# Performance work log

Hardware: AMD Instinct MI355X
Metric: run time of the kernel (lower is better)

## Reference

```python
import jax, jax.numpy as jnp
import numpy as np

N, C = 131072, 1000
ALPHA_LINK = 0.25  # weight applied when pred is a 'linked' (acceptable) confusion of gt
GAMMA = 2.0        # focal exponent


def setup_inputs() -> dict:
    key = jax.random.key(0)
    k1, k2, k3, k4 = jax.random.split(key, 4)
    y_pred = jax.random.normal(k1, (N, C), dtype=jnp.float32)
    y_true = jax.random.randint(k2, (N,), 0, C, dtype=jnp.int64)
    # Dense representation of the python link dict: link_matrix[gt, pred] == True
    # iff pred is in link[gt]; has_link[gt] == True iff gt is a key of link.
    link_matrix = jax.random.bernoulli(k3, 0.01, (C, C))
    has_link = jax.random.bernoulli(k4, 0.5, (C,))
    return {"y_pred": y_pred, "y_true": y_true,
            "link_matrix": link_matrix, "has_link": has_link}


def reference(y_pred, y_true, link_matrix, has_link):
    # per-sample cross entropy (stable log-softmax + gather)
    logp = jax.nn.log_softmax(y_pred, axis=-1)                     # [N, C]
    ce = -jnp.take_along_axis(logp, y_true[:, None], axis=1)[:, 0]  # [N]
    pt = jnp.exp(-ce)                                              # [N]
    pred = jnp.argmax(y_pred, axis=1)                              # [N]
    # link_bad: ALPHA_LINK iff pred != gt, gt in link, and pred in link[gt]; else 1
    linked = link_matrix[y_true, pred] & has_link[y_true] & (pred != y_true)
    w = jnp.where(linked, jnp.float32(ALPHA_LINK), jnp.float32(1.0))
    return jnp.mean(w * (1.0 - pt) ** GAMMA * ce)
```

## Files before the change

### kernel.cpp

```cpp
#include <hip/hip_runtime.h>
#include <math.h>


#define NROWS 131072
#define NC 1000
#define NF4 250
#define ROWS_PER_WAVE 4
#define WAVES_PER_BLOCK 4
#define ROWS_PER_BLOCK (ROWS_PER_WAVE * WAVES_PER_BLOCK)
#define NBLOCKS (NROWS / ROWS_PER_BLOCK)
#define NWAVES (NBLOCKS * WAVES_PER_BLOCK)
#define ALPHA_LINK 0.25f

__device__ __forceinline__ void load_row(const float4* __restrict__ rowp,
                                         int lane, float4 v[4]) {
    v[0] = rowp[lane];
    v[1] = rowp[lane + 64];
    v[2] = rowp[lane + 128];
    v[3] = (lane + 192 < NF4) ? rowp[lane + 192]
         : make_float4(-INFINITY, -INFINITY, -INFINITY, -INFINITY);
}

__global__ __launch_bounds__(256) void lfl_main(
    const float* __restrict__ yp,
    const int* __restrict__ yt,
    const unsigned char* __restrict__ linkb, const int* __restrict__ linki,
    const unsigned char* __restrict__ hasb,  const int* __restrict__ hasi,
    const unsigned int* __restrict__ hlw,
    float* __restrict__ partial)
{
    const int lane  = threadIdx.x & 63;
    const int wid   = threadIdx.x >> 6;
    const int gwave = blockIdx.x * WAVES_PER_BLOCK + wid;

    const int hi = yt[2 * lane + 1];
    const int y64 = (__ballot(hi != 0) == 0ULL);
    const unsigned int h0 = hlw[lane];
    const unsigned int h1 = hlw[lane + 64];
    const unsigned int h2 = hlw[lane + 128];
    const unsigned int h3 = (lane + 192 < NF4) ? hlw[lane + 192] : 0u;
    const int bfmt = (__ballot((h0 > 1u) | (h1 > 1u) | (h2 > 1u) | (h3 > 1u)) != 0ULL);

    const int row0 = blockIdx.x * ROWS_PER_BLOCK + wid * ROWS_PER_WAVE;
    float wsum = 0.0f;

    float4 v[4];
    load_row((const float4*)(yp + (size_t)row0 * NC), lane, v);

    #pragma unroll
    for (int r = 0; r < ROWS_PER_WAVE; ++r) {
        const int row = row0 + r;
        const int target = y64 ? yt[2 * row] : yt[row];
        const int tf = target >> 2;
        const int tl = target & 3;

        float4 vn[4];
        if (r + 1 < ROWS_PER_WAVE)
            load_row((const float4*)(yp + (size_t)(row + 1) * NC), lane, vn);

        float m = -INFINITY;
        int   idx = 1 << 30;
        float xt = 0.0f;
        #pragma unroll
        for (int k = 0; k < 4; ++k) {
            const int f  = lane + 64 * k;
            const int c0 = f * 4;
            const float x0 = v[k].x, x1 = v[k].y, x2 = v[k].z, x3 = v[k].w;
            if (x0 > m) { m = x0; idx = c0; }
            if (x1 > m) { m = x1; idx = c0 + 1; }
            if (x2 > m) { m = x2; idx = c0 + 2; }
            if (x3 > m) { m = x3; idx = c0 + 3; }
            if (f == tf) xt = (tl == 0) ? x0 : (tl == 1) ? x1 : (tl == 2) ? x2 : x3;
        }

        float s = 0.0f;
        #pragma unroll
        for (int k = 0; k < 4; ++k) {
            s += __expf(v[k].x - m) + __expf(v[k].y - m)
               + __expf(v[k].z - m) + __expf(v[k].w - m);
        }

        const float xts = __shfl(xt, tf & 63);

        #pragma unroll
        for (int off = 32; off; off >>= 1) {
            const float om = __shfl_xor(m, off);
            const int   oi = __shfl_xor(idx, off);
            const float os = __shfl_xor(s, off);
            const float mn = fmaxf(m, om);
            s = s * __expf(m - mn) + os * __expf(om - mn);
            if (om > m || (om == m && oi < idx)) idx = oi;
            m = mn;
        }

        const float logp_t = xts - m - __logf(s);
        const float ce = -logp_t;
        const float pt = __expf(logp_t);
        const int pred = idx;

        const size_t ofs = (size_t)target * NC + (size_t)pred;
        const bool lm = bfmt ? (linkb[ofs] != 0)    : (linki[ofs] != 0);
        const bool hb = bfmt ? (hasb[target] != 0)  : (hasi[target] != 0);
        const float w = (lm && hb && (pred != target)) ? ALPHA_LINK : 1.0f;

        const float ompt = 1.0f - pt;
        wsum += w * ompt * ompt * ce;

        if (r + 1 < ROWS_PER_WAVE) {
            v[0] = vn[0]; v[1] = vn[1]; v[2] = vn[2]; v[3] = vn[3];
        }
    }

    if (lane == 0) partial[gwave] = wsum;
}

__global__ __launch_bounds__(1024) void lfl_final(const float* __restrict__ partial,
                                                  float* __restrict__ out) {
    __shared__ float sm[1024];
    float s = 0.0f;
    for (int i = threadIdx.x; i < NWAVES; i += 1024) s += partial[i];
    sm[threadIdx.x] = s;
    __syncthreads();
    for (int stride = 512; stride; stride >>= 1) {
        if ((int)threadIdx.x < stride) sm[threadIdx.x] += sm[threadIdx.x + stride];
        __syncthreads();
    }
    if (threadIdx.x == 0) out[0] = sm[0] * (1.0f / (float)NROWS);
}

extern "C" void kernel_launch(void* const* d_in, const int* in_sizes, int n_in,
                              void* d_out, int out_size, void* d_ws, size_t ws_size,
                              hipStream_t stream) {
    const float* yp = (const float*)d_in[0];
    const int*   yt = (const int*)d_in[1];
    const void*  lk = d_in[2];
    const void*  hl = d_in[3];

    float* partial = (float*)d_ws;

    lfl_main<<<NBLOCKS, 256, 0, stream>>>(
        yp, yt,
        (const unsigned char*)lk, (const int*)lk,
        (const unsigned char*)hl, (const int*)hl,
        (const unsigned int*)hl,
        partial);
    lfl_final<<<1, 1024, 0, stream>>>(partial, (float*)d_out);
}
```

Measured before the change: 116.8 us.

## Issue all row loads up front and interleave per-row reductions

Each wave now issues every row's logit loads at kernel start as nontemporal loads, and loads the labels for both label formats eagerly instead of one row at a time. It then computes the row maxima and exp-sums, and runs the cross-lane shuffle reductions for all four rows interleaved. The goal is to put more memory requests in flight per wave and to hide shuffle latency across independent rows. In exchange, register pressure rises (64 floats of logits per lane), which the launch-bounds occupancy hint of 4 has to accommodate, and the unused label array is always read.

```diff
diff --git a/kernel.cpp b/kernel.cpp
--- a/kernel.cpp
+++ b/kernel.cpp
@@ -12,16 +12,9 @@
 #define NWAVES (NBLOCKS * WAVES_PER_BLOCK)
 #define ALPHA_LINK 0.25f
 
-__device__ __forceinline__ void load_row(const float4* __restrict__ rowp,
-                                         int lane, float4 v[4]) {
-    v[0] = rowp[lane];
-    v[1] = rowp[lane + 64];
-    v[2] = rowp[lane + 128];
-    v[3] = (lane + 192 < NF4) ? rowp[lane + 192]
-         : make_float4(-INFINITY, -INFINITY, -INFINITY, -INFINITY);
-}
+typedef float floatx4 __attribute__((ext_vector_type(4)));
 
-__global__ __launch_bounds__(256) void lfl_main(
+__global__ __launch_bounds__(256, 4) void lfl_main(
     const float* __restrict__ yp,
     const int* __restrict__ yt,
     const unsigned char* __restrict__ linkb, const int* __restrict__ linki,
@@ -32,83 +25,98 @@
     const int lane  = threadIdx.x & 63;
     const int wid   = threadIdx.x >> 6;
     const int gwave = blockIdx.x * WAVES_PER_BLOCK + wid;
+    const int row0  = blockIdx.x * ROWS_PER_BLOCK + wid * ROWS_PER_WAVE;
 
-    const int hi = yt[2 * lane + 1];
-    const int y64 = (__ballot(hi != 0) == 0ULL);
+    const int det_hi = yt[2 * lane + 1];
     const unsigned int h0 = hlw[lane];
     const unsigned int h1 = hlw[lane + 64];
     const unsigned int h2 = hlw[lane + 128];
     const unsigned int h3 = (lane + 192 < NF4) ? hlw[lane + 192] : 0u;
+    int t32[ROWS_PER_WAVE], t64[ROWS_PER_WAVE];
+    #pragma unroll
+    for (int r = 0; r < ROWS_PER_WAVE; ++r) {
+        t32[r] = yt[row0 + r];
+        t64[r] = yt[2 * (row0 + r)];
+    }
+
+    floatx4 v[ROWS_PER_WAVE][4];
+    #pragma unroll
+    for (int r = 0; r < ROWS_PER_WAVE; ++r) {
+        const floatx4* rowp = (const floatx4*)(yp + (size_t)(row0 + r) * NC);
+        v[r][0] = __builtin_nontemporal_load(rowp + lane);
+        v[r][1] = __builtin_nontemporal_load(rowp + lane + 64);
+        v[r][2] = __builtin_nontemporal_load(rowp + lane + 128);
+        if (lane + 192 < NF4) v[r][3] = __builtin_nontemporal_load(rowp + lane + 192);
+        else v[r][3] = (floatx4){-INFINITY, -INFINITY, -INFINITY, -INFINITY};
+    }
+
+    const int y64  = (__ballot(det_hi != 0) == 0ULL);
     const int bfmt = (__ballot((h0 > 1u) | (h1 > 1u) | (h2 > 1u) | (h3 > 1u)) != 0ULL);
 
-    const int row0 = blockIdx.x * ROWS_PER_BLOCK + wid * ROWS_PER_WAVE;
-    float wsum = 0.0f;
-
-    float4 v[4];
-    load_row((const float4*)(yp + (size_t)row0 * NC), lane, v);
-
+    int tgt[ROWS_PER_WAVE], tf[ROWS_PER_WAVE], tl[ROWS_PER_WAVE];
     #pragma unroll
     for (int r = 0; r < ROWS_PER_WAVE; ++r) {
-        const int row = row0 + r;
-        const int target = y64 ? yt[2 * row] : yt[row];
-        const int tf = target >> 2;
-        const int tl = target & 3;
+        tgt[r] = y64 ? t64[r] : t32[r];
+        tf[r] = tgt[r] >> 2;
+        tl[r] = tgt[r] & 3;
+    }
 
-        float4 vn[4];
-        if (r + 1 < ROWS_PER_WAVE)
-            load_row((const float4*)(yp + (size_t)(row + 1) * NC), lane, vn);
-
-        float m = -INFINITY;
-        int   idx = 1 << 30;
-        float xt = 0.0f;
+    float m[ROWS_PER_WAVE], xt[ROWS_PER_WAVE], s[ROWS_PER_WAVE];
+    int idx[ROWS_PER_WAVE];
+    #pragma unroll
+    for (int r = 0; r < ROWS_PER_WAVE; ++r) {
+        float mm = -INFINITY; int ii = 1 << 30; float xx = 0.0f;
         #pragma unroll
         for (int k = 0; k < 4; ++k) {
             const int f  = lane + 64 * k;
             const int c0 = f * 4;
-            const float x0 = v[k].x, x1 = v[k].y, x2 = v[k].z, x3 = v[k].w;
-            if (x0 > m) { m = x0; idx = c0; }
-            if (x1 > m) { m = x1; idx = c0 + 1; }
-            if (x2 > m) { m = x2; idx = c0 + 2; }
-            if (x3 > m) { m = x3; idx = c0 + 3; }
-            if (f == tf) xt = (tl == 0) ? x0 : (tl == 1) ? x1 : (tl == 2) ? x2 : x3;
+            const float x0 = v[r][k].x, x1 = v[r][k].y, x2 = v[r][k].z, x3 = v[r][k].w;
+            if (x0 > mm) { mm = x0; ii = c0; }
+            if (x1 > mm) { mm = x1; ii = c0 + 1; }
+            if (x2 > mm) { mm = x2; ii = c0 + 2; }
+            if (x3 > mm) { mm = x3; ii = c0 + 3; }
+            if (f == tf[r]) xx = (tl[r] == 0) ? x0 : (tl[r] == 1) ? x1 : (tl[r] == 2) ? x2 : x3;
         }
-
-        float s = 0.0f;
+        float ss = 0.0f;
         #pragma unroll
         for (int k = 0; k < 4; ++k) {
-            s += __expf(v[k].x - m) + __expf(v[k].y - m)
-               + __expf(v[k].z - m) + __expf(v[k].w - m);
+            ss += __expf(v[r][k].x - mm) + __expf(v[r][k].y - mm)
+                + __expf(v[r][k].z - mm) + __expf(v[r][k].w - mm);
         }
+        m[r] = mm; idx[r] = ii; xt[r] = xx; s[r] = ss;
+    }
 
-        const float xts = __shfl(xt, tf & 63);
+    float xts[ROWS_PER_WAVE];
+    #pragma unroll
+    for (int r = 0; r < ROWS_PER_WAVE; ++r) xts[r] = __shfl(xt[r], tf[r] & 63);
 
+    #pragma unroll
+    for (int off = 32; off; off >>= 1) {
         #pragma unroll
-        for (int off = 32; off; off >>= 1) {
-            const float om = __shfl_xor(m, off);
-            const int   oi = __shfl_xor(idx, off);
-            const float os = __shfl_xor(s, off);
-            const float mn = fmaxf(m, om);
-            s = s * __expf(m - mn) + os * __expf(om - mn);
-            if (om > m || (om == m && oi < idx)) idx = oi;
-            m = mn;
+        for (int r = 0; r < ROWS_PER_WAVE; ++r) {
+            const float om = __shfl_xor(m[r], off);
+            const int   oi = __shfl_xor(idx[r], off);
+            const float os = __shfl_xor(s[r], off);
+            const float mn = fmaxf(m[r], om);
+            s[r] = s[r] * __expf(m[r] - mn) + os * __expf(om - mn);
+            if (om > m[r] || (om == m[r] && oi < idx[r])) idx[r] = oi;
+            m[r] = mn;
         }
+    }
 
-        const float logp_t = xts - m - __logf(s);
+    float wsum = 0.0f;
+    #pragma unroll
+    for (int r = 0; r < ROWS_PER_WAVE; ++r) {
+        const float logp_t = xts[r] - m[r] - __logf(s[r]);
         const float ce = -logp_t;
         const float pt = __expf(logp_t);
-        const int pred = idx;
-
-        const size_t ofs = (size_t)target * NC + (size_t)pred;
+        const int pred = idx[r];
+        const size_t ofs = (size_t)tgt[r] * NC + (size_t)pred;
         const bool lm = bfmt ? (linkb[ofs] != 0)    : (linki[ofs] != 0);
-        const bool hb = bfmt ? (hasb[target] != 0)  : (hasi[target] != 0);
-        const float w = (lm && hb && (pred != target)) ? ALPHA_LINK : 1.0f;
-
+        const bool hb = bfmt ? (hasb[tgt[r]] != 0)  : (hasi[tgt[r]] != 0);
+        const float w = (lm && hb && (pred != tgt[r])) ? ALPHA_LINK : 1.0f;
         const float ompt = 1.0f - pt;
         wsum += w * ompt * ompt * ce;
-
-        if (r + 1 < ROWS_PER_WAVE) {
-            v[0] = vn[0]; v[1] = vn[1]; v[2] = vn[2]; v[3] = vn[3];
-        }
     }
 
     if (lane == 0) partial[gwave] = wsum;
```

After: 102.3 us, median of 2. 12.5% less time.
